# Kernel optimization log

Measured on AMD Instinct MI355X. Metric: run time of the kernel, lower is better.

## Reference

```python
import jax, jax.numpy as jnp
import numpy as np

A, B, T, D, UNITS = 4, 16, 1024, 1024, 1024

def setup_inputs() -> dict:
    key = jax.random.key(0)
    ks = jax.random.split(key, 8)
    scale_w5 = 1.0 / np.sqrt(D)
    scale_w6 = 1.0 / np.sqrt(D)
    scale_v = 1.0 / np.sqrt(UNITS)
    return {
        "query": jax.random.normal(ks[0], (B, D), dtype=jnp.float32),
        "value": jax.random.normal(ks[1], (A, B, T, D), dtype=jnp.float32),
        "W5_w": jax.random.normal(ks[2], (D, UNITS), dtype=jnp.float32) * scale_w5,
        "W5_b": jnp.zeros((UNITS,), dtype=jnp.float32),
        "W6_w": jax.random.normal(ks[3], (D, UNITS), dtype=jnp.float32) * scale_w6,
        "W6_b": jnp.zeros((UNITS,), dtype=jnp.float32),
        "V_w": jax.random.normal(ks[4], (UNITS, 1), dtype=jnp.float32) * scale_v,
        "V_b": jnp.zeros((1,), dtype=jnp.float32),
    }

def reference(query, value, W5_w, W5_b, W6_w, W6_b, V_w, V_b):
    # query: [B, D] -> expand to [B, 1, UNITS] after W6, broadcasts over T and agents
    qproj = query @ W6_w + W6_b                      # [B, UNITS]
    qproj = qproj[None, :, None, :]                  # [1, B, 1, UNITS]
    # W5 over every agent token: [A, B, T, UNITS]
    h = jnp.tanh(jnp.einsum('abtd,du->abtu', value, W5_w) + W5_b + qproj)
    # V -> scores [A, B, T, 1]; NOTE: original applies Softmax(axis=-1) over the
    # size-1 last axis (faithfully reproduced), which yields all-ones weights.
    scores = jnp.einsum('abtu,uo->abto', h, V_w) + V_b   # [A, B, T, 1]
    l = jax.nn.softmax(scores, axis=-1)                  # [A, B, T, 1]
    c = jnp.sum(l * value, axis=2)                       # [A, B, D], reduce over T
    return jnp.transpose(c, (1, 0, 2))                   # stack agents on axis=1 -> [B, A, D]
```

## Files before the change

kernel.cpp:

```cpp
#include <hip/hip_runtime.h>


constexpr int A_ = 4, B_ = 16, T_ = 1024, D_ = 1024;
constexpr int NCH  = 4;
constexpr int CHW  = D_ / NCH;
constexpr int NG   = 16;
constexpr int GT   = CHW / 4;
constexpr int ROWS = T_ / NG;
constexpr int STRIDE4 = D_ / 4;

__global__ __launch_bounds__(1024) void wa_fused(const float* __restrict__ value,
                                                 float* __restrict__ out) {
    const int blk = blockIdx.x;
    const int ch  = blk % NCH;
    const int ab  = blk / NCH;
    const int a   = ab / B_;
    const int b   = ab % B_;
    const int t   = threadIdx.x % GT;
    const int g   = threadIdx.x / GT;

    const float4* vp = reinterpret_cast<const float4*>(
        value + (size_t)ab * T_ * D_ + (size_t)g * ROWS * D_ + (size_t)ch * CHW) + t;

    float4 a0{0.f,0.f,0.f,0.f}, a1{0.f,0.f,0.f,0.f};
    float4 a2{0.f,0.f,0.f,0.f}, a3{0.f,0.f,0.f,0.f};
    for (int r = 0; r < ROWS; r += 4) {
        float4 v0 = vp[(size_t)(r + 0) * STRIDE4];
        float4 v1 = vp[(size_t)(r + 1) * STRIDE4];
        float4 v2 = vp[(size_t)(r + 2) * STRIDE4];
        float4 v3 = vp[(size_t)(r + 3) * STRIDE4];
        a0.x += v0.x; a0.y += v0.y; a0.z += v0.z; a0.w += v0.w;
        a1.x += v1.x; a1.y += v1.y; a1.z += v1.z; a1.w += v1.w;
        a2.x += v2.x; a2.y += v2.y; a2.z += v2.z; a2.w += v2.w;
        a3.x += v3.x; a3.y += v3.y; a3.z += v3.z; a3.w += v3.w;
    }
    float4 s;
    s.x = (a0.x + a1.x) + (a2.x + a3.x);
    s.y = (a0.y + a1.y) + (a2.y + a3.y);
    s.z = (a0.z + a1.z) + (a2.z + a3.z);
    s.w = (a0.w + a1.w) + (a2.w + a3.w);

    __shared__ float4 lds[NG * GT];
    lds[g * GT + t] = s;
    __syncthreads();
    #pragma unroll
    for (int sg = NG / 2; sg >= 1; sg >>= 1) {
        if (g < sg) {
            float4 o = lds[(g + sg) * GT + t];
            float4 m = lds[g * GT + t];
            m.x += o.x; m.y += o.y; m.z += o.z; m.w += o.w;
            lds[g * GT + t] = m;
        }
        __syncthreads();
    }
    if (g == 0) {
        reinterpret_cast<float4*>(
            out + ((size_t)(b * A_ + a)) * D_ + (size_t)ch * CHW)[t] = lds[t];
    }
}

extern "C" void kernel_launch(void* const* d_in, const int* in_sizes, int n_in,
                              void* d_out, int out_size, void* d_ws, size_t ws_size,
                              hipStream_t stream) {
    const float* value = (const float*)d_in[1];
    float* out = (float*)d_out;
    wa_fused<<<A_ * B_ * NCH, 1024, 0, stream>>>(value, out);
}
```

Measured before the change: 42.97 us.

## Split T reduction into two passes with full-row coalesced reads via workspace

Replaces the single fused column-chunk reduction with a pass that has each block sum a quarter of the T rows across the full D width, writing partials to workspace. A second small kernel adds the four partials per (agent, batch) into the output. This makes each block read whole contiguous rows and is meant to improve memory access efficiency. It adds a second launch and workspace traffic, and falls back to the old kernel if the workspace is too small.

After: 45.48 us. +5.8%, slower.

```diff
diff --git a/kernel.cpp b/kernel.cpp
--- a/kernel.cpp
+++ b/kernel.cpp
@@ -2,33 +2,30 @@
 
 
 constexpr int A_ = 4, B_ = 16, T_ = 1024, D_ = 1024;
-constexpr int NCH  = 4;
-constexpr int CHW  = D_ / NCH;
-constexpr int NG   = 16;
-constexpr int GT   = CHW / 4;
-constexpr int ROWS = T_ / NG;
-constexpr int STRIDE4 = D_ / 4;
+constexpr int NQ   = 4;
+constexpr int QROW = T_ / NQ;
+constexpr int NG   = 4;
+constexpr int GROW = QROW / NG;
+constexpr int D4   = D_ / 4;
 
-__global__ __launch_bounds__(1024) void wa_fused(const float* __restrict__ value,
-                                                 float* __restrict__ out) {
+__global__ __launch_bounds__(1024) void wa_pass1(const float* __restrict__ value,
+                                                 float* __restrict__ ws) {
     const int blk = blockIdx.x;
-    const int ch  = blk % NCH;
-    const int ab  = blk / NCH;
-    const int a   = ab / B_;
-    const int b   = ab % B_;
-    const int t   = threadIdx.x % GT;
-    const int g   = threadIdx.x / GT;
+    const int q   = blk % NQ;
+    const int ab  = blk / NQ;
+    const int t4  = threadIdx.x & (D4 - 1);
+    const int g   = threadIdx.x >> 8;
 
     const float4* vp = reinterpret_cast<const float4*>(
-        value + (size_t)ab * T_ * D_ + (size_t)g * ROWS * D_ + (size_t)ch * CHW) + t;
+        value + (size_t)ab * T_ * D_ + (size_t)(q * QROW + g * GROW) * D_) + t4;
 
     float4 a0{0.f,0.f,0.f,0.f}, a1{0.f,0.f,0.f,0.f};
     float4 a2{0.f,0.f,0.f,0.f}, a3{0.f,0.f,0.f,0.f};
-    for (int r = 0; r < ROWS; r += 4) {
-        float4 v0 = vp[(size_t)(r + 0) * STRIDE4];
-        float4 v1 = vp[(size_t)(r + 1) * STRIDE4];
-        float4 v2 = vp[(size_t)(r + 2) * STRIDE4];
-        float4 v3 = vp[(size_t)(r + 3) * STRIDE4];
+    for (int r = 0; r < GROW; r += 4) {
+        float4 v0 = vp[(size_t)(r + 0) * D4];
+        float4 v1 = vp[(size_t)(r + 1) * D4];
+        float4 v2 = vp[(size_t)(r + 2) * D4];
+        float4 v3 = vp[(size_t)(r + 3) * D4];
         a0.x += v0.x; a0.y += v0.y; a0.z += v0.z; a0.w += v0.w;
         a1.x += v1.x; a1.y += v1.y; a1.z += v1.z; a1.w += v1.w;
         a2.x += v2.x; a2.y += v2.y; a2.z += v2.z; a2.w += v2.w;
@@ -40,11 +37,73 @@
     s.z = (a0.z + a1.z) + (a2.z + a3.z);
     s.w = (a0.w + a1.w) + (a2.w + a3.w);
 
-    __shared__ float4 lds[NG * GT];
+    __shared__ float4 lds[NG * D4];
+    lds[threadIdx.x] = s;
+    __syncthreads();
+    if (g < 2) {
+        float4 o = lds[threadIdx.x + 2 * D4];
+        float4 m = lds[threadIdx.x];
+        m.x += o.x; m.y += o.y; m.z += o.z; m.w += o.w;
+        lds[threadIdx.x] = m;
+    }
+    __syncthreads();
+    if (g == 0) {
+        float4 o = lds[t4 + D4];
+        float4 m = lds[t4];
+        m.x += o.x; m.y += o.y; m.z += o.z; m.w += o.w;
+        reinterpret_cast<float4*>(ws + (size_t)blk * D_)[t4] = m;
+    }
+}
+
+__global__ __launch_bounds__(256) void wa_pass2(const float* __restrict__ ws,
+                                                float* __restrict__ out) {
+    const int ab = blockIdx.x;
+    const int a  = ab / B_;
+    const int b  = ab % B_;
+    const int t4 = threadIdx.x;
+    float4 acc{0.f,0.f,0.f,0.f};
+    #pragma unroll
+    for (int q = 0; q < NQ; ++q) {
+        float4 v = reinterpret_cast<const float4*>(ws + (size_t)(ab * NQ + q) * D_)[t4];
+        acc.x += v.x; acc.y += v.y; acc.z += v.z; acc.w += v.w;
+    }
+    reinterpret_cast<float4*>(out + (size_t)(b * A_ + a) * D_)[t4] = acc;
+}
+
+constexpr int NCH = 4, CHW = D_ / NCH, NGf = 16, GT = CHW / 4, ROWS = T_ / NGf;
+__global__ __launch_bounds__(1024) void wa_fused(const float* __restrict__ value,
+                                                 float* __restrict__ out) {
+    const int blk = blockIdx.x;
+    const int ch  = blk % NCH;
+    const int ab  = blk / NCH;
+    const int a   = ab / B_;
+    const int b   = ab % B_;
+    const int t   = threadIdx.x % GT;
+    const int g   = threadIdx.x / GT;
+    const float4* vp = reinterpret_cast<const float4*>(
+        value + (size_t)ab * T_ * D_ + (size_t)g * ROWS * D_ + (size_t)ch * CHW) + t;
+    float4 a0{0.f,0.f,0.f,0.f}, a1{0.f,0.f,0.f,0.f};
+    float4 a2{0.f,0.f,0.f,0.f}, a3{0.f,0.f,0.f,0.f};
+    for (int r = 0; r < ROWS; r += 4) {
+        float4 v0 = vp[(size_t)(r + 0) * (D_ / 4)];
+        float4 v1 = vp[(size_t)(r + 1) * (D_ / 4)];
+        float4 v2 = vp[(size_t)(r + 2) * (D_ / 4)];
+        float4 v3 = vp[(size_t)(r + 3) * (D_ / 4)];
+        a0.x += v0.x; a0.y += v0.y; a0.z += v0.z; a0.w += v0.w;
+        a1.x += v1.x; a1.y += v1.y; a1.z += v1.z; a1.w += v1.w;
+        a2.x += v2.x; a2.y += v2.y; a2.z += v2.z; a2.w += v2.w;
+        a3.x += v3.x; a3.y += v3.y; a3.z += v3.z; a3.w += v3.w;
+    }
+    float4 s;
+    s.x = (a0.x + a1.x) + (a2.x + a3.x);
+    s.y = (a0.y + a1.y) + (a2.y + a3.y);
+    s.z = (a0.z + a1.z) + (a2.z + a3.z);
+    s.w = (a0.w + a1.w) + (a2.w + a3.w);
+    __shared__ float4 lds[NGf * GT];
     lds[g * GT + t] = s;
     __syncthreads();
     #pragma unroll
-    for (int sg = NG / 2; sg >= 1; sg >>= 1) {
+    for (int sg = NGf / 2; sg >= 1; sg >>= 1) {
         if (g < sg) {
             float4 o = lds[(g + sg) * GT + t];
             float4 m = lds[g * GT + t];
@@ -53,10 +112,8 @@
         }
         __syncthreads();
     }
-    if (g == 0) {
-        reinterpret_cast<float4*>(
-            out + ((size_t)(b * A_ + a)) * D_ + (size_t)ch * CHW)[t] = lds[t];
-    }
+    if (g == 0)
+        reinterpret_cast<float4*>(out + (size_t)(b * A_ + a) * D_ + (size_t)ch * CHW)[t] = lds[t];
 }
 
 extern "C" void kernel_launch(void* const* d_in, const int* in_sizes, int n_in,
@@ -64,5 +121,12 @@
                               hipStream_t stream) {
     const float* value = (const float*)d_in[1];
     float* out = (float*)d_out;
-    wa_fused<<<A_ * B_ * NCH, 1024, 0, stream>>>(value, out);
+    const size_t need = (size_t)A_ * B_ * NQ * D_ * sizeof(float);
+    if (ws_size >= need) {
+        float* ws = (float*)d_ws;
+        wa_pass1<<<A_ * B_ * NQ, 1024, 0, stream>>>(value, ws);
+        wa_pass2<<<A_ * B_, 256, 0, stream>>>(ws, out);
+    } else {
+        wa_fused<<<A_ * B_ * NCH, 1024, 0, stream>>>(value, out);
+    }
 }
```
